# Kernel optimization log

Hardware: AMD Instinct MI355X
Metric: run time of the kernel (lower is better)

The kernel has to match this reference:

```python
import jax, jax.numpy as jnp
import numpy as np


def setup_inputs() -> dict:
    key = jax.random.key(0)
    k1, k2 = jax.random.split(key)
    bsz, beam_size = 64, 8
    R = bsz * beam_size  # 512 rows
    step = 511
    seq_len = step + 1
    vocab = 50257
    n = 3
    tokens = jax.random.randint(k1, (R, seq_len), 0, 100, dtype=jnp.int64)
    lprobs = jax.random.normal(k2, (R, vocab), dtype=jnp.float32)
    return {
        "tokens": tokens,
        "lprobs": lprobs,
        "bsz": bsz,
        "step": step,
        "beam_size": beam_size,
        "no_repeat_ngram_size": n,
    }


def reference(tokens, lprobs, bsz, step, beam_size, no_repeat_ngram_size):
    # tokens: (bsz*beam, seq_len) int; lprobs: (bsz*beam, vocab) float
    n = no_repeat_ngram_size
    R, V = lprobs.shape
    num_starts = step - n + 2  # number of historical n-gram start positions
    if num_starts < 1:
        return lprobs
    starts = jnp.arange(num_starts)
    # windows of the first (n-1) tokens of each historical n-gram: (R, S, n-1)
    win_idx = starts[:, None] + jnp.arange(n - 1)
    windows = tokens[:, win_idx]
    # current (n-1)-token suffix ending at `step`: (R, n-1)
    suffix = tokens[:, step - n + 2 : step + 1]
    match = jnp.all(windows == suffix[:, None, :], axis=-1)  # (R, S)
    banned = tokens[:, starts + n - 1]  # token completing each matched n-gram
    rows = jnp.arange(R)[:, None]
    ban_mask = jnp.zeros((R, V), dtype=bool).at[rows, banned].max(match)
    return jnp.where(ban_mask, -jnp.inf, lprobs)
```

## Files before the change

### kernel.cpp

```cpp
#include <hip/hip_runtime.h>


#define BAN_VALUE (-3.3895313892515355e+38f)

__global__ void copy_f4_kernel(const float4* __restrict__ in,
                               float4* __restrict__ out, int n4) {
    int i = blockIdx.x * blockDim.x + threadIdx.x;
    if (i < n4) out[i] = in[i];
}

__global__ void ban_kernel(const int* __restrict__ tokens,
                           const int* __restrict__ step_p,
                           const int* __restrict__ n_p,
                           float* __restrict__ out,
                           int seq_len, int V) {
    const int row  = blockIdx.x;
    const int step = *step_p;
    const int n    = *n_p;
    const int num_starts = step - n + 2;
    if (num_starts < 1) return;

    bool is64 = true;
    for (int k = 1; k < 64; k += 2) {
        if (tokens[k] != 0) { is64 = false; break; }
    }
    const long long* t64 = (const long long*)tokens;
    const int*       t32 = tokens;
    const long base = (long)row * seq_len;

    #define TOK(i) (is64 ? (int)t64[base + (i)] : t32[base + (i)])

    const int suf0 = step - n + 2;

    for (int s = threadIdx.x; s < num_starts; s += blockDim.x) {
        bool match = true;
        for (int j = 0; j < n - 1; ++j) {
            if (TOK(s + j) != TOK(suf0 + j)) { match = false; break; }
        }
        if (match) {
            int banned = TOK(s + n - 1);
            if (banned < 0) banned = 0;
            if (banned >= V) banned = V - 1;
            out[(long)row * V + banned] = BAN_VALUE;
        }
    }
    #undef TOK
}

extern "C" void kernel_launch(void* const* d_in, const int* in_sizes, int n_in,
                              void* d_out, int out_size, void* d_ws, size_t ws_size,
                              hipStream_t stream) {
    const int*   tokens = (const int*)d_in[0];
    const float* lprobs = (const float*)d_in[1];
    const int* step_p = (const int*)d_in[3];
    const int* n_p    = (const int*)d_in[5];
    float* out = (float*)d_out;

    const int R = 512;
    const int seq_len = in_sizes[0] / R;
    const int V = out_size / R;

    const int n4 = out_size / 4;
    const int threads = 256;
    const int blocks = (n4 + threads - 1) / threads;
    copy_f4_kernel<<<blocks, threads, 0, stream>>>(
        (const float4*)lprobs, (float4*)out, n4);

    ban_kernel<<<R, 256, 0, stream>>>(tokens, step_p, n_p, out, seq_len, V);
}
```

Baseline: 190.5 us.

## Fuse lprobs copy and n-gram banning into one per-row kernel

```diff
diff --git a/kernel.cpp b/kernel.cpp
--- a/kernel.cpp
+++ b/kernel.cpp
@@ -2,49 +2,111 @@
 
 
 #define BAN_VALUE (-3.3895313892515355e+38f)
+#define MAXB 640
 
-__global__ void copy_f4_kernel(const float4* __restrict__ in,
-                               float4* __restrict__ out, int n4) {
-    int i = blockIdx.x * blockDim.x + threadIdx.x;
-    if (i < n4) out[i] = in[i];
-}
-
-__global__ void ban_kernel(const int* __restrict__ tokens,
-                           const int* __restrict__ step_p,
-                           const int* __restrict__ n_p,
-                           float* __restrict__ out,
-                           int seq_len, int V) {
+__global__ __launch_bounds__(1024, 8)
+void fused_ban_copy(const int* __restrict__ tokens,
+                    const int* __restrict__ step_p,
+                    const int* __restrict__ n_p,
+                    const float* __restrict__ lprobs,
+                    float* __restrict__ out,
+                    int seq_len, int V) {
     const int row  = blockIdx.x;
+    const int tid  = threadIdx.x;
     const int step = *step_p;
     const int n    = *n_p;
     const int num_starts = step - n + 2;
-    if (num_starts < 1) return;
 
-    bool is64 = true;
-    for (int k = 1; k < 64; k += 2) {
-        if (tokens[k] != 0) { is64 = false; break; }
+    __shared__ int s_is64;
+    __shared__ int s_cnt;
+    __shared__ int tok[1024];
+    __shared__ int list[MAXB];
+
+    if (tid == 0) s_cnt = 0;
+    if (tid < 64) {
+        bool oddnz = false;
+        if (tid < 32) oddnz = tokens[2 * tid + 1] != 0;
+        bool any64 = __any(oddnz);
+        if (tid == 0) s_is64 = any64 ? 0 : 1;
     }
+    __syncthreads();
+
+    const bool is64 = (s_is64 != 0);
     const long long* t64 = (const long long*)tokens;
-    const int*       t32 = tokens;
-    const long base = (long)row * seq_len;
+    const long rowTok = (long)row * seq_len;
 
-    #define TOK(i) (is64 ? (int)t64[base + (i)] : t32[base + (i)])
+    const bool do_ban  = (num_starts >= 1) && (n >= 1);
+    const bool use_lds = do_ban && (step < 1024);
 
-    const int suf0 = step - n + 2;
+    #define GTOK(i) (is64 ? (int)t64[rowTok + (i)] : tokens[rowTok + (i)])
 
-    for (int s = threadIdx.x; s < num_starts; s += blockDim.x) {
-        bool match = true;
-        for (int j = 0; j < n - 1; ++j) {
-            if (TOK(s + j) != TOK(suf0 + j)) { match = false; break; }
+    if (do_ban) {
+        if (use_lds) {
+            for (int t = tid; t <= step; t += (int)blockDim.x)
+                tok[t] = GTOK(t);
+            __syncthreads();
         }
-        if (match) {
-            int banned = TOK(s + n - 1);
-            if (banned < 0) banned = 0;
-            if (banned >= V) banned = V - 1;
-            out[(long)row * V + banned] = BAN_VALUE;
+        const int suf0 = step - n + 2;
+        for (int s = tid; s < num_starts; s += (int)blockDim.x) {
+            bool match = true;
+            for (int j = 0; j < n - 1; ++j) {
+                const int a = use_lds ? tok[s + j]    : GTOK(s + j);
+                const int b = use_lds ? tok[suf0 + j] : GTOK(suf0 + j);
+                if (a != b) { match = false; break; }
+            }
+            if (match) {
+                int banned = use_lds ? tok[s + n - 1] : GTOK(s + n - 1);
+                if (banned < 0) banned = 0;
+                if (banned >= V) banned = V - 1;
+                const int pos = atomicAdd(&s_cnt, 1);
+                if (pos < MAXB) list[pos] = banned;
+            }
         }
+        __syncthreads();
     }
-    #undef TOK
+    #undef GTOK
+
+    const int cnt = do_ban ? (s_cnt < MAXB ? s_cnt : MAXB) : 0;
+
+    const long rowbase = (long)row * V;
+    const float* __restrict__ in_row  = lprobs + rowbase;
+    float*       __restrict__ out_row = out + rowbase;
+
+    int pad = (int)((-rowbase) & 3);
+    if (pad > V) pad = V;
+    const int K     = (V - pad) >> 2;
+    const int tail0 = pad + (K << 2);
+
+    const float4* __restrict__ in4  = (const float4*)(in_row + pad);
+    float4*       __restrict__ out4 = (float4*)(out_row + pad);
+
+    for (int q = tid; q < K; q += (int)blockDim.x) {
+        float4 v = in4[q];
+        if (cnt) {
+            const int c0 = pad + (q << 2);
+            for (int e = 0; e < cnt; ++e) {
+                const int d = list[e] - c0;
+                v.x = (d == 0) ? BAN_VALUE : v.x;
+                v.y = (d == 1) ? BAN_VALUE : v.y;
+                v.z = (d == 2) ? BAN_VALUE : v.z;
+                v.w = (d == 3) ? BAN_VALUE : v.w;
+            }
+        }
+        out4[q] = v;
+    }
+
+    int c = -1;
+    if (tid < 4) {
+        if (tid < pad) c = tid;
+    } else if (tid < 8) {
+        const int t = tail0 + (tid - 4);
+        if (t < V) c = t;
+    }
+    if (c >= 0) {
+        float v = in_row[c];
+        for (int e = 0; e < cnt; ++e) v = (list[e] == c) ? BAN_VALUE : v;
+        out_row[c] = v;
+    }
 }
 
 extern "C" void kernel_launch(void* const* d_in, const int* in_sizes, int n_in,
@@ -60,11 +122,6 @@
     const int seq_len = in_sizes[0] / R;
     const int V = out_size / R;
 
-    const int n4 = out_size / 4;
-    const int threads = 256;
-    const int blocks = (n4 + threads - 1) / threads;
-    copy_f4_kernel<<<blocks, threads, 0, stream>>>(
-        (const float4*)lprobs, (float4*)out, n4);
-
-    ban_kernel<<<R, 256, 0, stream>>>(tokens, step_p, n_p, out, seq_len, V);
+    fused_ban_copy<<<R, 1024, 0, stream>>>(tokens, step_p, n_p,
+                                           lprobs, out, seq_len, V);
 }
```

After: 200.8 us. 1.05x slower.
